# Optimization experiments

Measured on AMD Instinct MI355X. Metric: run time of the kernel, lower is better.

## Reference

```python
import jax, jax.numpy as jnp
import numpy as np
import math

B, L, C, H, W = 2, 8, 64, 64, 33
M1, M2 = 16, 16


def setup_inputs() -> dict:
    key = jax.random.key(0)
    ks = jax.random.split(key, 6)
    scale = 1.0 / math.sqrt(C)
    shp_x = (B, L, C, H, W)
    shp_w = (C, C, M1, M2)
    return {
        "x_real": jax.random.normal(ks[0], shp_x, jnp.float32),
        "x_imag": jax.random.normal(ks[1], shp_x, jnp.float32),
        "wr1": scale * jax.random.normal(ks[2], shp_w, jnp.float32),
        "wi1": scale * jax.random.normal(ks[3], shp_w, jnp.float32),
        "wr2": scale * jax.random.normal(ks[4], shp_w, jnp.float32),
        "wi2": scale * jax.random.normal(ks[5], shp_w, jnp.float32),
    }


def _cmul_einsum(xr, xi, wr, wi):
    # complex einsum 'blcxy,ocxy->bloxy' expressed in real arithmetic
    or_ = jnp.einsum('blcxy,ocxy->bloxy', xr, wr) - jnp.einsum('blcxy,ocxy->bloxy', xi, wi)
    oi_ = jnp.einsum('blcxy,ocxy->bloxy', xr, wi) + jnp.einsum('blcxy,ocxy->bloxy', xi, wr)
    return or_, oi_


def reference(x_real, x_imag, wr1, wi1, wr2, wi2):
    m1 = min(H, M1)
    m2 = min(W, M2)
    # corner 1: low positive frequencies
    o1r, o1i = _cmul_einsum(x_real[:, :, :, :m1, :m2], x_imag[:, :, :, :m1, :m2],
                            wr1[:, :, :m1, :m2], wi1[:, :, :m1, :m2])
    out_r = jnp.zeros((B, L, C, H, W), jnp.float32).at[:, :, :, :m1, :m2].set(o1r)
    out_i = jnp.zeros((B, L, C, H, W), jnp.float32).at[:, :, :, :m1, :m2].set(o1i)
    if H > 1:
        # corner 2: high (negative) frequencies along H
        o2r, o2i = _cmul_einsum(x_real[:, :, :, -m1:, :m2], x_imag[:, :, :, -m1:, :m2],
                                wr2[:, :, :m1, :m2], wi2[:, :, :m1, :m2])
        out_r = out_r.at[:, :, :, -m1:, :m2].set(o2r)
        out_i = out_i.at[:, :, :, -m1:, :m2].set(o2i)
    # stack real/imag (equivalent to the complex output of the torch module)
    return jnp.stack([out_r, out_i], axis=0)
```

## Files before the change

### kernel.cpp

```cpp
#include <hip/hip_runtime.h>


constexpr int Cc    = 64;
constexpr int Ww    = 33;
constexpr int HW    = 64 * Ww;
constexpr int PLANE = Cc * HW;
constexpr int TOT   = 16 * PLANE;
constexpr int WSTR  = Cc * 16 * 16;

#define CFMA(AR, AI, A, B, WRE, WIM)                                \
    AR.x = fmaf(A.x, WRE.x, AR.x); AR.x = fmaf(-B.x, WIM.x, AR.x); \
    AI.x = fmaf(A.x, WIM.x, AI.x); AI.x = fmaf( B.x, WRE.x, AI.x); \
    AR.y = fmaf(A.y, WRE.y, AR.y); AR.y = fmaf(-B.y, WIM.y, AR.y); \
    AI.y = fmaf(A.y, WIM.y, AI.y); AI.y = fmaf( B.y, WRE.y, AI.y); \
    AR.z = fmaf(A.z, WRE.z, AR.z); AR.z = fmaf(-B.z, WIM.z, AR.z); \
    AI.z = fmaf(A.z, WIM.z, AI.z); AI.z = fmaf( B.z, WRE.z, AI.z); \
    AR.w = fmaf(A.w, WRE.w, AR.w); AR.w = fmaf(-B.w, WIM.w, AR.w); \
    AI.w = fmaf(A.w, WIM.w, AI.w); AI.w = fmaf( B.w, WRE.w, AI.w);

__global__ __launch_bounds__(256) void spectral_fused_kernel(
    const float* __restrict__ xr, const float* __restrict__ xi,
    const float* __restrict__ wr1, const float* __restrict__ wi1,
    const float* __restrict__ wr2, const float* __restrict__ wi2,
    float* __restrict__ out)
{
    const int bid = blockIdx.x;
    const int t   = threadIdx.x;

    if (bid < 512) {
        const int oq     = bid & 3;
        const int blq    = (bid >> 2) & 3;
        const int xrow   = (bid >> 4) & 15;
        const int corner = bid >> 8;
        const int xin    = corner ? (48 + xrow) : xrow;
        const float* wr  = corner ? wr2 : wr1;
        const float* wi  = corner ? wi2 : wi1;

        __shared__ __align__(16) float xs[8192];

        {
            const int y  = t & 15;
            const int wb = (t >> 4) & 3;
            const int cg = t >> 6;
            const int src_base = (blq * 4 + wb) * PLANE + xin * Ww + y;
            #pragma unroll
            for (int k = 0; k < 32; ++k) {
                const int r = k >> 4;
                const int c = ((k & 15) << 2) | cg;
                const float* src = (r ? xi : xr) + (size_t)src_base + c * HW;
                xs[r * 4096 + c * 64 + wb * 16 + y] = *src;
            }
        }
        __syncthreads();

        const int yq = t & 3;
        const int bp = (t >> 2) & 1;
        const int op = (t >> 3) & 7;
        const int ch = t >> 6;
        const int o0 = oq * 16 + op * 2;
        const int cb = ch * 16;

        const float* wrp = wr + o0 * WSTR + xrow * 16 + yq * 4;
        const float* wip = wi + o0 * WSTR + xrow * 16 + yq * 4;
        const float4* xsr = reinterpret_cast<const float4*>(xs) + bp * 8 + yq;
        const float4* xsi = xsr + 1024;

        float4 ar[2][2], ai[2][2];
        #pragma unroll
        for (int i = 0; i < 2; ++i)
            #pragma unroll
            for (int j = 0; j < 2; ++j) {
                ar[i][j] = make_float4(0.f, 0.f, 0.f, 0.f);
                ai[i][j] = make_float4(0.f, 0.f, 0.f, 0.f);
            }

        #pragma unroll 4
        for (int cc = 0; cc < 16; ++cc) {
            const int c = cb + cc;
            float4 wre[2], wim[2], a[2], b[2];
            #pragma unroll
            for (int i = 0; i < 2; ++i) {
                wre[i] = *reinterpret_cast<const float4*>(wrp + i * WSTR + c * 256);
                wim[i] = *reinterpret_cast<const float4*>(wip + i * WSTR + c * 256);
            }
            #pragma unroll
            for (int j = 0; j < 2; ++j) {
                a[j] = xsr[c * 16 + j * 4];
                b[j] = xsi[c * 16 + j * 4];
            }
            CFMA(ar[0][0], ai[0][0], a[0], b[0], wre[0], wim[0])
            CFMA(ar[0][1], ai[0][1], a[1], b[1], wre[0], wim[0])
            CFMA(ar[1][0], ai[1][0], a[0], b[0], wre[1], wim[1])
            CFMA(ar[1][1], ai[1][1], a[1], b[1], wre[1], wim[1])
        }

        __syncthreads();
        const int cfg = t & 63;
        if (ch) {
            float4* sc = reinterpret_cast<float4*>(xs) + ((ch - 1) * 64 + cfg) * 9;
            #pragma unroll
            for (int i = 0; i < 2; ++i)
                #pragma unroll
                for (int j = 0; j < 2; ++j) {
                    sc[i * 2 + j]     = ar[i][j];
                    sc[4 + i * 2 + j] = ai[i][j];
                }
        }
        __syncthreads();
        if (!ch) {
            #pragma unroll
            for (int p = 0; p < 3; ++p) {
                const float4* sc = reinterpret_cast<const float4*>(xs)
                                 + ((p * 64 + cfg) * 9);
                #pragma unroll
                for (int i = 0; i < 2; ++i)
                    #pragma unroll
                    for (int j = 0; j < 2; ++j) {
                        const float4 pr = sc[i * 2 + j];
                        const float4 pi = sc[4 + i * 2 + j];
                        ar[i][j].x += pr.x; ar[i][j].y += pr.y;
                        ar[i][j].z += pr.z; ar[i][j].w += pr.w;
                        ai[i][j].x += pi.x; ai[i][j].y += pi.y;
                        ai[i][j].z += pi.z; ai[i][j].w += pi.w;
                    }
            }
            #pragma unroll
            for (int i = 0; i < 2; ++i)
                #pragma unroll
                for (int j = 0; j < 2; ++j) {
                    const int o  = o0 + i;
                    const int bl = blq * 4 + bp * 2 + j;
                    const size_t ob = (size_t)(bl * Cc + o) * HW
                                    + (size_t)xin * Ww + yq * 4;
                    out[ob + 0] = ar[i][j].x; out[ob + 1] = ar[i][j].y;
                    out[ob + 2] = ar[i][j].z; out[ob + 3] = ar[i][j].w;
                    out[TOT + ob + 0] = ai[i][j].x; out[TOT + ob + 1] = ai[i][j].y;
                    out[TOT + ob + 2] = ai[i][j].z; out[TOT + ob + 3] = ai[i][j].w;
                }
        }

        #pragma unroll
        for (int q = 0; q < 9; ++q) {
            const int k = t + q * 256;
            if (k < 2176) {
                const int ri   = k >= 1088;
                const int rem  = ri ? (k - 1088) : k;
                const int ol_  = rem / 68;
                const int sub  = rem - ol_ * 68;
                const int blj_ = sub / 17;
                const int yy   = 16 + (sub - blj_ * 17);
                const size_t idx = (size_t)((blq * 4 + blj_) * Cc + oq * 16 + ol_) * HW
                                 + (size_t)xin * Ww + yy + (ri ? (size_t)TOT : 0);
                out[idx] = 0.f;
            }
        }
    } else {
        const int p     = bid - 512;
        const int ri    = p >> 10;
        const int plane = p & 1023;
        float4* dst = (float4*)(out + (size_t)ri * TOT + (size_t)plane * HW + 528);
        const float4 z = make_float4(0.f, 0.f, 0.f, 0.f);
        dst[t] = z;
        if (t < 8) dst[256 + t] = z;
    }
}

extern "C" void kernel_launch(void* const* d_in, const int* in_sizes, int n_in,
                              void* d_out, int out_size, void* d_ws, size_t ws_size,
                              hipStream_t stream) {
    const float* xr  = (const float*)d_in[0];
    const float* xi  = (const float*)d_in[1];
    const float* wr1 = (const float*)d_in[2];
    const float* wi1 = (const float*)d_in[3];
    const float* wr2 = (const float*)d_in[4];
    const float* wi2 = (const float*)d_in[5];
    float* out = (float*)d_out;

    spectral_fused_kernel<<<2560, 256, 0, stream>>>(xr, xi, wr1, wi1, wr2, wi2, out);
}
```

Measured before the change: 94.48 us.

## Double block size to 512 threads, sharing weights across 16 batch-time slices

Each compute block now covers 16 batch-time slices instead of 4 for a given output quarter and frequency row. It uses 512 threads and twice the shared memory, so each weight load is reused across more inputs and global weight traffic drops by half. The cross-channel reduction now spreads across all threads with a coalesced shared-memory layout, so a quarter of the threads no longer do it alone. The zero-fill blocks each clear two planes. The trade-off is half as many compute blocks (256), which may underfill the GPU, plus 64KB of shared memory per block.

```diff
diff --git a/kernel.cpp b/kernel.cpp
--- a/kernel.cpp
+++ b/kernel.cpp
@@ -18,7 +18,7 @@
     AR.w = fmaf(A.w, WRE.w, AR.w); AR.w = fmaf(-B.w, WIM.w, AR.w); \
     AI.w = fmaf(A.w, WIM.w, AI.w); AI.w = fmaf( B.w, WRE.w, AI.w);
 
-__global__ __launch_bounds__(256) void spectral_fused_kernel(
+__global__ __launch_bounds__(512, 2) void spectral_fused_kernel(
     const float* __restrict__ xr, const float* __restrict__ xi,
     const float* __restrict__ wr1, const float* __restrict__ wi1,
     const float* __restrict__ wr2, const float* __restrict__ wi2,
@@ -27,43 +27,43 @@
     const int bid = blockIdx.x;
     const int t   = threadIdx.x;
 
-    if (bid < 512) {
+    if (bid < 256) {
         const int oq     = bid & 3;
-        const int blq    = (bid >> 2) & 3;
-        const int xrow   = (bid >> 4) & 15;
-        const int corner = bid >> 8;
+        const int blg    = (bid >> 2) & 1;
+        const int xrow   = (bid >> 3) & 15;
+        const int corner = bid >> 7;
         const int xin    = corner ? (48 + xrow) : xrow;
         const float* wr  = corner ? wr2 : wr1;
         const float* wi  = corner ? wi2 : wi1;
 
-        __shared__ __align__(16) float xs[8192];
+        __shared__ __align__(16) float xs[16384];
 
         {
             const int y  = t & 15;
-            const int wb = (t >> 4) & 3;
-            const int cg = t >> 6;
-            const int src_base = (blq * 4 + wb) * PLANE + xin * Ww + y;
+            const int wb = (t >> 4) & 7;
+            const int cg = t >> 7;
+            const int src_base = (blg * 8 + wb) * PLANE + xin * Ww + y;
             #pragma unroll
             for (int k = 0; k < 32; ++k) {
                 const int r = k >> 4;
                 const int c = ((k & 15) << 2) | cg;
                 const float* src = (r ? xi : xr) + (size_t)src_base + c * HW;
-                xs[r * 4096 + c * 64 + wb * 16 + y] = *src;
+                xs[r * 8192 + c * 128 + wb * 16 + y] = *src;
             }
         }
         __syncthreads();
 
-        const int yq = t & 3;
-        const int bp = (t >> 2) & 1;
-        const int op = (t >> 3) & 7;
-        const int ch = t >> 6;
-        const int o0 = oq * 16 + op * 2;
-        const int cb = ch * 16;
+        const int yq  = t & 3;
+        const int bls = (t >> 2) & 3;
+        const int ops = (t >> 4) & 7;
+        const int ch  = t >> 7;
+        const int o0  = oq * 16 + ops * 2;
+        const int cb  = ch * 16;
 
         const float* wrp = wr + o0 * WSTR + xrow * 16 + yq * 4;
         const float* wip = wi + o0 * WSTR + xrow * 16 + yq * 4;
-        const float4* xsr = reinterpret_cast<const float4*>(xs) + bp * 8 + yq;
-        const float4* xsi = xsr + 1024;
+        const float4* xsr = reinterpret_cast<const float4*>(xs) + bls * 8 + yq;
+        const float4* xsi = xsr + 2048;
 
         float4 ar[2][2], ai[2][2];
         #pragma unroll
@@ -85,8 +85,8 @@
             }
             #pragma unroll
             for (int j = 0; j < 2; ++j) {
-                a[j] = xsr[c * 16 + j * 4];
-                b[j] = xsi[c * 16 + j * 4];
+                a[j] = xsr[c * 32 + j * 4];
+                b[j] = xsi[c * 32 + j * 4];
             }
             CFMA(ar[0][0], ai[0][0], a[0], b[0], wre[0], wim[0])
             CFMA(ar[0][1], ai[0][1], a[1], b[1], wre[0], wim[0])
@@ -95,73 +95,77 @@
         }
 
         __syncthreads();
-        const int cfg = t & 63;
-        if (ch) {
-            float4* sc = reinterpret_cast<float4*>(xs) + ((ch - 1) * 64 + cfg) * 9;
+        {
+            float4* sc = reinterpret_cast<float4*>(xs);
+            const int tile = t & 127;
             #pragma unroll
-            for (int i = 0; i < 2; ++i)
-                #pragma unroll
-                for (int j = 0; j < 2; ++j) {
-                    sc[i * 2 + j]     = ar[i][j];
-                    sc[4 + i * 2 + j] = ai[i][j];
-                }
+            for (int k2 = 0; k2 < 8; ++k2) {
+                const int kk = k2 & 3;
+                const int i  = kk >> 1, j = kk & 1;
+                const float4 v = (k2 < 4) ? ar[i][j] : ai[i][j];
+                sc[ch * 1024 + k2 * 128 + tile] = v;
+            }
         }
         __syncthreads();
-        if (!ch) {
+
+        {
+            const float4* sc = reinterpret_cast<const float4*>(xs);
             #pragma unroll
-            for (int p = 0; p < 3; ++p) {
-                const float4* sc = reinterpret_cast<const float4*>(xs)
-                                 + ((p * 64 + cfg) * 9);
+            for (int q = 0; q < 2; ++q) {
+                const int m    = t + q * 512;
+                const int tile = m & 127;
+                const int k    = m >> 7;
+                float4 acc = sc[k * 128 + tile];
                 #pragma unroll
-                for (int i = 0; i < 2; ++i)
-                    #pragma unroll
-                    for (int j = 0; j < 2; ++j) {
-                        const float4 pr = sc[i * 2 + j];
-                        const float4 pi = sc[4 + i * 2 + j];
-                        ar[i][j].x += pr.x; ar[i][j].y += pr.y;
-                        ar[i][j].z += pr.z; ar[i][j].w += pr.w;
-                        ai[i][j].x += pi.x; ai[i][j].y += pi.y;
-                        ai[i][j].z += pi.z; ai[i][j].w += pi.w;
-                    }
+                for (int p = 1; p < 4; ++p) {
+                    const float4 pr = sc[p * 1024 + k * 128 + tile];
+                    acc.x += pr.x; acc.y += pr.y; acc.z += pr.z; acc.w += pr.w;
+                }
+                const int yq_  = tile & 3;
+                const int bls_ = (tile >> 2) & 3;
+                const int ops_ = (tile >> 4) & 7;
+                const int ri   = k >> 2;
+                const int kk   = k & 3;
+                const int o    = oq * 16 + ops_ * 2 + (kk >> 1);
+                const int bl   = blg * 8 + bls_ * 2 + (kk & 1);
+                const size_t ob = (size_t)(bl * Cc + o) * HW
+                                + (size_t)xin * Ww + yq_ * 4
+                                + (ri ? (size_t)TOT : 0);
+                out[ob + 0] = acc.x; out[ob + 1] = acc.y;
+                out[ob + 2] = acc.z; out[ob + 3] = acc.w;
             }
-            #pragma unroll
-            for (int i = 0; i < 2; ++i)
-                #pragma unroll
-                for (int j = 0; j < 2; ++j) {
-                    const int o  = o0 + i;
-                    const int bl = blq * 4 + bp * 2 + j;
-                    const size_t ob = (size_t)(bl * Cc + o) * HW
-                                    + (size_t)xin * Ww + yq * 4;
-                    out[ob + 0] = ar[i][j].x; out[ob + 1] = ar[i][j].y;
-                    out[ob + 2] = ar[i][j].z; out[ob + 3] = ar[i][j].w;
-                    out[TOT + ob + 0] = ai[i][j].x; out[TOT + ob + 1] = ai[i][j].y;
-                    out[TOT + ob + 2] = ai[i][j].z; out[TOT + ob + 3] = ai[i][j].w;
-                }
         }
 
         #pragma unroll
         for (int q = 0; q < 9; ++q) {
-            const int k = t + q * 256;
-            if (k < 2176) {
-                const int ri   = k >= 1088;
-                const int rem  = ri ? (k - 1088) : k;
-                const int ol_  = rem / 68;
-                const int sub  = rem - ol_ * 68;
+            const int k = t + q * 512;
+            if (k < 4352) {
+                const int ri   = k >= 2176;
+                const int rem  = ri ? (k - 2176) : k;
+                const int ol_  = rem / 136;
+                const int sub  = rem - ol_ * 136;
                 const int blj_ = sub / 17;
                 const int yy   = 16 + (sub - blj_ * 17);
-                const size_t idx = (size_t)((blq * 4 + blj_) * Cc + oq * 16 + ol_) * HW
+                const size_t idx = (size_t)((blg * 8 + blj_) * Cc + oq * 16 + ol_) * HW
                                  + (size_t)xin * Ww + yy + (ri ? (size_t)TOT : 0);
                 out[idx] = 0.f;
             }
         }
     } else {
-        const int p     = bid - 512;
-        const int ri    = p >> 10;
-        const int plane = p & 1023;
-        float4* dst = (float4*)(out + (size_t)ri * TOT + (size_t)plane * HW + 528);
+        const int p = bid - 256;
         const float4 z = make_float4(0.f, 0.f, 0.f, 0.f);
-        dst[t] = z;
-        if (t < 8) dst[256 + t] = z;
+        #pragma unroll
+        for (int q = 0; q < 2; ++q) {
+            const int j = t + q * 512;
+            if (j < 528) {
+                const int pl  = p * 2 + (j >= 264);
+                const int off = j - (j >= 264 ? 264 : 0);
+                const int ri  = pl >> 10;
+                float4* dst = (float4*)(out + (size_t)ri * TOT
+                                            + (size_t)(pl & 1023) * HW + 528);
+                dst[off] = z;
+            }
+        }
     }
 }
 
@@ -176,5 +180,5 @@
     const float* wi2 = (const float*)d_in[5];
     float* out = (float*)d_out;
 
-    spectral_fused_kernel<<<2560, 256, 0, stream>>>(xr, xi, wr1, wi1, wr2, wi2, out);
+    spectral_fused_kernel<<<1280, 512, 0, stream>>>(xr, xi, wr1, wi1, wr2, wi2, out);
 }
```

New measurement: 93.89 us. Within noise of the previous version (-0.6%).

## Software-pipeline weight/LDS loads and parallelize cross-warp reduction over all threads

Applied to the files above, without the earlier changes.

The channel loop is fully unrolled and uses register ring buffers: weights are prefetched four channels ahead from global memory and x values two channels ahead from LDS, so load latency overlaps the complex FMAs. The split-K reduction now has every channel group write its partials to LDS in a conflict-free layout, and all 256 threads each reduce and store two float4 results, where before one quarter of the threads did the whole reduction. launch_bounds is raised to a minimum of 2 blocks per CU. The prefetch buffers raise register pressure, and the occupancy hint may force spills.

```diff
diff --git a/kernel.cpp b/kernel.cpp
--- a/kernel.cpp
+++ b/kernel.cpp
@@ -18,7 +18,7 @@
     AR.w = fmaf(A.w, WRE.w, AR.w); AR.w = fmaf(-B.w, WIM.w, AR.w); \
     AI.w = fmaf(A.w, WIM.w, AI.w); AI.w = fmaf( B.w, WRE.w, AI.w);
 
-__global__ __launch_bounds__(256) void spectral_fused_kernel(
+__global__ __launch_bounds__(256, 2) void spectral_fused_kernel(
     const float* __restrict__ xr, const float* __restrict__ xi,
     const float* __restrict__ wr1, const float* __restrict__ wi1,
     const float* __restrict__ wr2, const float* __restrict__ wi2,
@@ -74,69 +74,88 @@
                 ai[i][j] = make_float4(0.f, 0.f, 0.f, 0.f);
             }
 
-        #pragma unroll 4
+        float4 wreb[4][2], wimb[4][2], ab[2][2], bb[2][2];
+        #pragma unroll
+        for (int p = 0; p < 4; ++p) {
+            const int c = cb + p;
+            wreb[p][0] = *reinterpret_cast<const float4*>(wrp + c * 256);
+            wreb[p][1] = *reinterpret_cast<const float4*>(wrp + WSTR + c * 256);
+            wimb[p][0] = *reinterpret_cast<const float4*>(wip + c * 256);
+            wimb[p][1] = *reinterpret_cast<const float4*>(wip + WSTR + c * 256);
+        }
+        #pragma unroll
+        for (int p = 0; p < 2; ++p) {
+            const int c = cb + p;
+            ab[p][0] = xsr[c * 16];     ab[p][1] = xsr[c * 16 + 4];
+            bb[p][0] = xsi[c * 16];     bb[p][1] = xsi[c * 16 + 4];
+        }
+
+        #pragma unroll
         for (int cc = 0; cc < 16; ++cc) {
-            const int c = cb + cc;
-            float4 wre[2], wim[2], a[2], b[2];
-            #pragma unroll
-            for (int i = 0; i < 2; ++i) {
-                wre[i] = *reinterpret_cast<const float4*>(wrp + i * WSTR + c * 256);
-                wim[i] = *reinterpret_cast<const float4*>(wip + i * WSTR + c * 256);
+            const int ws = cc & 3;
+            const int xl = cc & 1;
+            const float4 wre0 = wreb[ws][0], wre1 = wreb[ws][1];
+            const float4 wim0 = wimb[ws][0], wim1 = wimb[ws][1];
+            const float4 a0 = ab[xl][0], a1 = ab[xl][1];
+            const float4 b0 = bb[xl][0], b1 = bb[xl][1];
+
+            if (cc + 4 < 16) {
+                const int c = cb + cc + 4;
+                wreb[ws][0] = *reinterpret_cast<const float4*>(wrp + c * 256);
+                wreb[ws][1] = *reinterpret_cast<const float4*>(wrp + WSTR + c * 256);
+                wimb[ws][0] = *reinterpret_cast<const float4*>(wip + c * 256);
+                wimb[ws][1] = *reinterpret_cast<const float4*>(wip + WSTR + c * 256);
             }
-            #pragma unroll
-            for (int j = 0; j < 2; ++j) {
-                a[j] = xsr[c * 16 + j * 4];
-                b[j] = xsi[c * 16 + j * 4];
+            if (cc + 2 < 16) {
+                const int c = cb + cc + 2;
+                ab[xl][0] = xsr[c * 16];    ab[xl][1] = xsr[c * 16 + 4];
+                bb[xl][0] = xsi[c * 16];    bb[xl][1] = xsi[c * 16 + 4];
             }
-            CFMA(ar[0][0], ai[0][0], a[0], b[0], wre[0], wim[0])
-            CFMA(ar[0][1], ai[0][1], a[1], b[1], wre[0], wim[0])
-            CFMA(ar[1][0], ai[1][0], a[0], b[0], wre[1], wim[1])
-            CFMA(ar[1][1], ai[1][1], a[1], b[1], wre[1], wim[1])
+
+            CFMA(ar[0][0], ai[0][0], a0, b0, wre0, wim0)
+            CFMA(ar[0][1], ai[0][1], a1, b1, wre0, wim0)
+            CFMA(ar[1][0], ai[1][0], a0, b0, wre1, wim1)
+            CFMA(ar[1][1], ai[1][1], a1, b1, wre1, wim1)
         }
 
         __syncthreads();
-        const int cfg = t & 63;
-        if (ch) {
-            float4* sc = reinterpret_cast<float4*>(xs) + ((ch - 1) * 64 + cfg) * 9;
+        {
+            float4* sc = reinterpret_cast<float4*>(xs);
+            const int tile = t & 63;
             #pragma unroll
-            for (int i = 0; i < 2; ++i)
-                #pragma unroll
-                for (int j = 0; j < 2; ++j) {
-                    sc[i * 2 + j]     = ar[i][j];
-                    sc[4 + i * 2 + j] = ai[i][j];
-                }
+            for (int k2 = 0; k2 < 8; ++k2) {
+                const int ri = k2 >> 2, i = (k2 >> 1) & 1, j = k2 & 1;
+                const float4 v = ri ? ai[i][j] : ar[i][j];
+                sc[ch * 512 + k2 * 64 + tile] = v;
+            }
         }
         __syncthreads();
-        if (!ch) {
+
+        {
+            const float4* sc = reinterpret_cast<const float4*>(xs);
             #pragma unroll
-            for (int p = 0; p < 3; ++p) {
-                const float4* sc = reinterpret_cast<const float4*>(xs)
-                                 + ((p * 64 + cfg) * 9);
+            for (int q = 0; q < 2; ++q) {
+                const int m    = t + q * 256;
+                const int tile = m & 63;
+                const int k2   = m >> 6;
+                float4 acc = sc[k2 * 64 + tile];
                 #pragma unroll
-                for (int i = 0; i < 2; ++i)
-                    #pragma unroll
-                    for (int j = 0; j < 2; ++j) {
-                        const float4 pr = sc[i * 2 + j];
-                        const float4 pi = sc[4 + i * 2 + j];
-                        ar[i][j].x += pr.x; ar[i][j].y += pr.y;
-                        ar[i][j].z += pr.z; ar[i][j].w += pr.w;
-                        ai[i][j].x += pi.x; ai[i][j].y += pi.y;
-                        ai[i][j].z += pi.z; ai[i][j].w += pi.w;
-                    }
+                for (int p = 1; p < 4; ++p) {
+                    const float4 pr = sc[p * 512 + k2 * 64 + tile];
+                    acc.x += pr.x; acc.y += pr.y; acc.z += pr.z; acc.w += pr.w;
+                }
+                const int yq_ = tile & 3;
+                const int bp_ = (tile >> 2) & 1;
+                const int op_ = (tile >> 3) & 7;
+                const int ri  = k2 >> 2;
+                const int o   = oq * 16 + op_ * 2 + ((k2 >> 1) & 1);
+                const int bl  = blq * 4 + bp_ * 2 + (k2 & 1);
+                const size_t ob = (size_t)(bl * Cc + o) * HW
+                                + (size_t)xin * Ww + yq_ * 4
+                                + (ri ? (size_t)TOT : 0);
+                out[ob + 0] = acc.x; out[ob + 1] = acc.y;
+                out[ob + 2] = acc.z; out[ob + 3] = acc.w;
             }
-            #pragma unroll
-            for (int i = 0; i < 2; ++i)
-                #pragma unroll
-                for (int j = 0; j < 2; ++j) {
-                    const int o  = o0 + i;
-                    const int bl = blq * 4 + bp * 2 + j;
-                    const size_t ob = (size_t)(bl * Cc + o) * HW
-                                    + (size_t)xin * Ww + yq * 4;
-                    out[ob + 0] = ar[i][j].x; out[ob + 1] = ar[i][j].y;
-                    out[ob + 2] = ar[i][j].z; out[ob + 3] = ar[i][j].w;
-                    out[TOT + ob + 0] = ai[i][j].x; out[TOT + ob + 1] = ai[i][j].y;
-                    out[TOT + ob + 2] = ai[i][j].z; out[TOT + ob + 3] = ai[i][j].w;
-                }
         }
 
         #pragma unroll
```

Measured after the change: 136.5 us. +44.5%, slower.
